# Kernel optimization log

Hardware: AMD Instinct MI355X
Metric: run time of the kernel (lower is better)

The kernel has to match this reference:

```python
import jax, jax.numpy as jnp
import numpy as np

B, S, D, H, DFF = 4, 2048, 768, 12, 3072
DH = D // H  # 64
EPS = 1e-5
SQRT_DK = float(np.sqrt(DH))


def layer_norm(x, gamma, beta):
    mu = jnp.mean(x, axis=-1, keepdims=True)
    var = jnp.mean((x - mu) ** 2, axis=-1, keepdims=True)
    return (x - mu) / jnp.sqrt(var + EPS) * gamma + beta


def attention_block(x, Wq, Wv, gamma, beta, mask):
    # NOTE: faithful to source quirks: k and v BOTH come from the V projection
    # (self.K is unused), and softmax is over dim=2 (the QUERY axis) as in
    # nn.Softmax(dim=2) applied to a (B, H, Sq, Sk) tensor.
    b, s, d = x.shape
    q = (x @ Wq).reshape(b, s, H, DH).transpose(0, 2, 1, 3)   # (B,H,S,DH)
    kv = (x @ Wv).reshape(b, s, H, DH).transpose(0, 2, 1, 3)  # (B,H,S,DH)
    w = jnp.einsum('bhqd,bhkd->bhqk', q, kv) / SQRT_DK        # (B,H,S,S)
    w = jnp.where(mask, -1e9, w)
    score = jax.nn.softmax(w, axis=2)  # dim=2 quirk (query axis)
    o = jnp.einsum('bhqk,bhkd->bhqd', score, kv)
    o = o.transpose(0, 2, 1, 3).reshape(b, s, d)
    return layer_norm(o + x, gamma, beta)


def feed_forward(x, W1, b1, W2, b2, gamma, beta):
    h = jax.nn.relu(x @ W1 + b1)
    return layer_norm(h @ W2 + b2 + x, gamma, beta)


def setup_inputs() -> dict:
    key = jax.random.key(0)
    ks = jax.random.split(key, 12)
    std = 1.0 / np.sqrt(D)
    x = jax.random.normal(ks[0], (B, S, D), dtype=jnp.float32)
    # causal mask: True = masked
    mask = jnp.triu(jnp.ones((S, S), dtype=bool), k=1)[None, None]
    return {
        'x': x,
        'mask': mask,
        'Wq1': jax.random.normal(ks[1], (D, D), jnp.float32) * std,
        'Wv1': jax.random.normal(ks[2], (D, D), jnp.float32) * std,
        'g1': jnp.ones((D,), jnp.float32),
        'be1': jnp.zeros((D,), jnp.float32),
        'Wq2': jax.random.normal(ks[3], (D, D), jnp.float32) * std,
        'Wv2': jax.random.normal(ks[4], (D, D), jnp.float32) * std,
        'g2': jnp.ones((D,), jnp.float32),
        'be2': jnp.zeros((D,), jnp.float32),
        'Wf1': jax.random.normal(ks[5], (D, DFF), jnp.float32) * std,
        'bf1': jnp.zeros((DFF,), jnp.float32),
        'Wf2': jax.random.normal(ks[6], (DFF, D), jnp.float32) * (1.0 / np.sqrt(DFF)),
        'bf2': jnp.zeros((D,), jnp.float32),
        'gf': jnp.ones((D,), jnp.float32),
        'bef': jnp.zeros((D,), jnp.float32),
    }


def reference(x, mask, Wq1, Wv1, g1, be1, Wq2, Wv2, g2, be2,
              Wf1, bf1, Wf2, bf2, gf, bef):
    x = attention_block(x, Wq1, Wv1, g1, be1, mask)
    # second block: mask is zeroed in the source (no masking)
    x = attention_block(x, Wq2, Wv2, g2, be2, jnp.zeros_like(mask))
    x = feed_forward(x, Wf1, bf1, Wf2, bf2, gf, bef)
    return x
```

## Files before the change

### kernel.cpp

```cpp
#include <hip/hip_runtime.h>

typedef __attribute__((ext_vector_type(8))) short short8;
typedef __attribute__((ext_vector_type(4))) float floatx4;
typedef __attribute__((ext_vector_type(4))) unsigned short ushort4v;

#define H_ 12
#define S_ 2048
#define D_ 768
#define DFF_ 3072
#define DH_ 64
#define BH_ 48
#define M_ 8192

__device__ __forceinline__ unsigned short f2bf(float f) {
  union { float f; unsigned int u; } a; a.f = f;
  return (unsigned short)((a.u + 0x7FFFu + ((a.u >> 16) & 1u)) >> 16);
}
__device__ __forceinline__ float bf2f(unsigned short s) {
  union { unsigned int u; float f; } a; a.u = ((unsigned int)s) << 16;
  return a.f;
}

__device__ __forceinline__ void glds16(const void* g, void* l) {
  __builtin_amdgcn_global_load_lds(
      (const __attribute__((address_space(1))) void*)(unsigned long long)(size_t)g,
      (__attribute__((address_space(3))) void*)(unsigned int)(size_t)l, 16, 0, 0);
}

__device__ __forceinline__ int swz8(int lin, int nwg) {
  return (lin & 7) * (nwg >> 3) + (lin >> 3);
}

__global__ __launch_bounds__(256) void cvt_bf16(const float* __restrict__ in,
                                                unsigned short* __restrict__ out) {
  size_t i = ((size_t)blockIdx.x * 256 + threadIdx.x) * 4;
  floatx4 v = *reinterpret_cast<const floatx4*>(in + i);
  ushort4v o;
  o[0] = f2bf(v[0]); o[1] = f2bf(v[1]); o[2] = f2bf(v[2]); o[3] = f2bf(v[3]);
  *reinterpret_cast<ushort4v*>(out + i) = o;
}

__global__ __launch_bounds__(256) void wtrans(const float* __restrict__ W,
                                              unsigned short* __restrict__ Wt,
                                              int K, int N) {
  __shared__ float t[64][65];
  const int n0 = blockIdx.x * 64, k0 = blockIdx.y * 64;
  const int tid = threadIdx.x;
#pragma unroll
  for (int i = 0; i < 16; ++i) {
    int idx = tid + 256 * i;
    int kl = idx >> 6, nl = idx & 63;
    t[kl][nl] = W[(size_t)(k0 + kl) * N + n0 + nl];
  }
  __syncthreads();
#pragma unroll
  for (int i = 0; i < 16; ++i) {
    int idx = tid + 256 * i;
    int nl = idx >> 6, kl = idx & 63;
    Wt[(size_t)(n0 + nl) * K + k0 + kl] = f2bf(t[kl][nl]);
  }
}

__global__ __launch_bounds__(256) void kvtrans(const unsigned short* __restrict__ KVb,
                                               unsigned short* __restrict__ KVTb) {
  __shared__ unsigned short t[64][72];
  const int kk0 = blockIdx.x * 64;
  const int bh = blockIdx.y, b = bh / H_, h = bh % H_;
  const size_t xbase = ((size_t)b * S_) * D_ + h * DH_;
  const int tid = threadIdx.x;
#pragma unroll
  for (int i = 0; i < 16; ++i) {
    int idx = tid + 256 * i;
    int kl = idx >> 6, d = idx & 63;
    t[kl][d] = KVb[xbase + (size_t)(kk0 + kl) * D_ + d];
  }
  __syncthreads();
  const size_t tb = (size_t)bh * DH_ * S_;
#pragma unroll
  for (int i = 0; i < 16; ++i) {
    int idx = tid + 256 * i;
    int d = idx >> 6, kl = idx & 63;
    KVTb[tb + (size_t)d * S_ + kk0 + kl] = t[kl][d];
  }
}

template <int EPI, int OUTBF>
__global__ __launch_bounds__(256, 2) void gemm128(const unsigned short* __restrict__ A,
                                                  const unsigned short* __restrict__ Bt,
                                                  const float* __restrict__ bias,
                                                  float scale, void* __restrict__ C0,
                                                  void* __restrict__ C1,
                                                  int M, int N, int K, int lda) {
  __shared__ unsigned short As[128 * 64];
  __shared__ unsigned short Bs[128 * 64];
  const int tid = threadIdx.x;
  const int l = tid & 63, w = tid >> 6;
  const int wm = w >> 1, wn = w & 1;
  const int lrow = l & 15, lk = l >> 4;
  int lin = (blockIdx.z * gridDim.y + blockIdx.y) * gridDim.x + blockIdx.x;
  int nwg = gridDim.x * gridDim.y * gridDim.z;
  int s = swz8(lin, nwg);
  int xt = s % gridDim.x;
  int rest = s / gridDim.x;
  int yt = rest % gridDim.y;
  int zt = rest / gridDim.y;
  const unsigned short* Ao = A + (size_t)zt * K;
  const unsigned short* Bo = Bt + (size_t)zt * K;
  const int m0 = yt * 128, n0 = xt * 128;
  floatx4 acc[4][4] = {};
  for (int k0 = 0; k0 < K; k0 += 64) {
    __syncthreads();
#pragma unroll
    for (int i = 0; i < 4; ++i) {
      int idx = w * 64 + i * 256 + l;
      int row = idx >> 3, c8 = idx & 7;
      int sc = (c8 ^ (row & 7)) << 3;
      glds16(Ao + (size_t)(m0 + row) * lda + k0 + sc, As + (size_t)(w * 64 + i * 256) * 8);
      glds16(Bo + (size_t)(n0 + row) * lda + k0 + sc, Bs + (size_t)(w * 64 + i * 256) * 8);
    }
    __syncthreads();
#pragma unroll
    for (int ks = 0; ks < 2; ++ks) {
      short8 af[4], bfr[4];
#pragma unroll
      for (int f = 0; f < 4; ++f) {
        int ar = wm * 64 + f * 16 + lrow;
        af[f] = *reinterpret_cast<const short8*>(
            &As[ar * 64 + (((ks * 4 + lk) ^ (ar & 7)) << 3)]);
        int br = wn * 64 + f * 16 + lrow;
        bfr[f] = *reinterpret_cast<const short8*>(
            &Bs[br * 64 + (((ks * 4 + lk) ^ (br & 7)) << 3)]);
      }
#pragma unroll
      for (int fm = 0; fm < 4; ++fm)
#pragma unroll
        for (int fn = 0; fn < 4; ++fn)
          acc[fm][fn] =
              __builtin_amdgcn_mfma_f32_16x16x32_bf16(af[fm], bfr[fn], acc[fm][fn], 0, 0, 0);
    }
  }
#pragma unroll
  for (int fm = 0; fm < 4; ++fm) {
#pragma unroll
    for (int fn = 0; fn < 4; ++fn) {
      int col = n0 + wn * 64 + fn * 16 + lrow;
#pragma unroll
      for (int r = 0; r < 4; ++r) {
        int row = m0 + wm * 64 + fm * 16 + lk * 4 + r;
        float v = acc[fm][fn][r];
        if (EPI == 3) {
          if (col < 768)
            ((unsigned short*)C0)[(size_t)row * 768 + col] = f2bf(v * scale);
          else
            ((unsigned short*)C1)[(size_t)row * 768 + col - 768] = f2bf(v);
        } else {
          v = v * scale + ((EPI > 0) ? bias[col] : 0.0f);
          if (EPI == 1) v = fmaxf(v, 0.0f);
          void* Cz = zt ? C1 : C0;
          if (OUTBF) ((unsigned short*)Cz)[(size_t)row * N + col] = f2bf(v);
          else ((float*)Cz)[(size_t)row * N + col] = v;
        }
      }
    }
  }
}

template <bool CAUSAL>
__global__ __launch_bounds__(256, 4) void colsum(const unsigned short* __restrict__ Qb,
                                                 const unsigned short* __restrict__ KVb,
                                                 float* __restrict__ lnl) {
  __shared__ unsigned short kvs[64 * 64];
  __shared__ float lred[4][64];
  const int tid = threadIdx.x;
  const int l = tid & 63, w = tid >> 6;
  const int lrow = l & 15, lk = l >> 4;
  const int sw = swz8(blockIdx.x, 32 * BH_);
  const int bh = sw >> 5, kt = sw & 31;
  const int kk0 = kt * 64;
  const int b = bh / H_, h = bh % H_;
  const size_t xbase = ((size_t)b * S_) * D_ + h * DH_;
#pragma unroll
  for (int i = 0; i < 2; ++i) {
    int idx = w * 64 + i * 256 + l;
    int row = idx >> 3, c8 = idx & 7;
    glds16(KVb + xbase + (size_t)(kk0 + row) * D_ + ((c8 ^ (row & 7)) << 3),
           kvs + (size_t)(w * 64 + i * 256) * 8);
  }
  __syncthreads();
  short8 bkv[4][2];
#pragma unroll
  for (int kkf = 0; kkf < 4; ++kkf)
#pragma unroll
    for (int s = 0; s < 2; ++s) {
      int br = kkf * 16 + lrow;
      bkv[kkf][s] = *reinterpret_cast<const short8*>(
          &kvs[br * 64 + (((s * 4 + lk) ^ (br & 7)) << 3)]);
    }
  float lrun[4] = {0.0f, 0.0f, 0.0f, 0.0f};
  const int qbase = CAUSAL ? kk0 : 0;
  const int ntiles = (S_ - qbase) >> 4;
  for (int t = w; t < ntiles; t += 4) {
    const int q0 = qbase + t * 16;
    const bool maskt = CAUSAL && (q0 < kk0 + 64);
    short8 aq[2];
#pragma unroll
    for (int s = 0; s < 2; ++s)
      aq[s] = *reinterpret_cast<const short8*>(
          &Qb[xbase + (size_t)(q0 + lrow) * D_ + s * 32 + lk * 8]);
#pragma unroll
    for (int kkf = 0; kkf < 4; ++kkf) {
      floatx4 sf = {};
      sf = __builtin_amdgcn_mfma_f32_16x16x32_bf16(aq[0], bkv[kkf][0], sf, 0, 0, 0);
      sf = __builtin_amdgcn_mfma_f32_16x16x32_bf16(aq[1], bkv[kkf][1], sf, 0, 0, 0);
      const int kkg = kk0 + kkf * 16 + lrow;
      float lacc = 0.0f;
      if (maskt) {
#pragma unroll
        for (int r = 0; r < 4; ++r) {
          int qg = q0 + lk * 4 + r;
          lacc += (kkg <= qg) ? __expf(sf[r]) : 0.0f;
        }
      } else {
#pragma unroll
        for (int r = 0; r < 4; ++r) lacc += __expf(sf[r]);
      }
      lrun[kkf] += lacc;
    }
  }
#pragma unroll
  for (int kkf = 0; kkf < 4; ++kkf) {
    float lv = lrun[kkf];
    lv += __shfl_xor(lv, 16, 64);
    lv += __shfl_xor(lv, 32, 64);
    if (l < 16) lred[w][kkf * 16 + l] = lv;
  }
  __syncthreads();
  if (tid < 64) {
    float lv = lred[0][tid] + lred[1][tid] + lred[2][tid] + lred[3][tid];
    lnl[(size_t)bh * S_ + kk0 + tid] = __logf(lv);
  }
}

template <bool CAUSAL>
__global__ __launch_bounds__(256, 4) void attnpv(const unsigned short* __restrict__ Qb,
                                                 const unsigned short* __restrict__ KVb,
                                                 const unsigned short* __restrict__ KVTb,
                                                 const float* __restrict__ lnl,
                                                 float* __restrict__ Opre) {
  __shared__ unsigned short kvs[64 * 64];
  __shared__ unsigned short kvts[64 * 64];
  __shared__ unsigned short ps[4][32 * 64];
  __shared__ float slnl[64];
  const int tid = threadIdx.x;
  const int l = tid & 63, w = tid >> 6;
  const int lrow = l & 15, lk = l >> 4;
  const int sw = swz8(blockIdx.x, 16 * BH_);
  const int bh = sw >> 4, qtr = sw & 15;
  const int qt = CAUSAL ? (15 - qtr) : qtr;
  const int q0 = qt * 128;
  const int wr = w * 32;
  const int b = bh / H_, h = bh % H_;
  const size_t xbase = ((size_t)b * S_) * D_ + h * DH_;
  const size_t tbase = (size_t)bh * DH_ * S_;
  short8 aq[2][2];
#pragma unroll
  for (int fm = 0; fm < 2; ++fm)
#pragma unroll
    for (int s = 0; s < 2; ++s)
      aq[fm][s] = *reinterpret_cast<const short8*>(
          &Qb[xbase + (size_t)(q0 + wr + fm * 16 + lrow) * D_ + s * 32 + lk * 8]);
  floatx4 ao[2][4] = {};
  const int nkk = CAUSAL ? 2 * (qt + 1) : (S_ / 64);
  for (int t = 0; t < nkk; ++t) {
    const int kk0 = t * 64;
    __syncthreads();
#pragma unroll
    for (int i = 0; i < 2; ++i) {
      int idx = w * 64 + i * 256 + l;
      int row = idx >> 3, c8 = idx & 7;
      int sc = (c8 ^ (row & 7)) << 3;
      glds16(KVb + xbase + (size_t)(kk0 + row) * D_ + sc,
             kvs + (size_t)(w * 64 + i * 256) * 8);
      glds16(KVTb + tbase + (size_t)row * S_ + kk0 + sc,
             kvts + (size_t)(w * 64 + i * 256) * 8);
    }
    if (tid < 64) slnl[tid] = lnl[(size_t)bh * S_ + kk0 + tid];
    __syncthreads();
    const bool maskt = CAUSAL && (kk0 + 64 > q0);
#pragma unroll
    for (int kkf = 0; kkf < 4; ++kkf) {
      const int kkl = kkf * 16 + lrow;
      const int br = kkf * 16 + lrow;
      short8 b0 = *reinterpret_cast<const short8*>(&kvs[br * 64 + ((lk ^ (br & 7)) << 3)]);
      short8 b1 =
          *reinterpret_cast<const short8*>(&kvs[br * 64 + (((4 + lk) ^ (br & 7)) << 3)]);
      const float nl = -slnl[kkl];
      const int kkg = kk0 + kkl;
#pragma unroll
      for (int fm = 0; fm < 2; ++fm) {
        floatx4 sf = {nl, nl, nl, nl};
        sf = __builtin_amdgcn_mfma_f32_16x16x32_bf16(aq[fm][0], b0, sf, 0, 0, 0);
        sf = __builtin_amdgcn_mfma_f32_16x16x32_bf16(aq[fm][1], b1, sf, 0, 0, 0);
#pragma unroll
        for (int r = 0; r < 4; ++r) {
          int prow = fm * 16 + lk * 4 + r;
          float p;
          if (maskt)
            p = (kkg <= q0 + wr + prow) ? __expf(sf[r]) : 0.0f;
          else
            p = __expf(sf[r]);
          ps[w][prow * 64 + (((kkl >> 3) ^ (prow & 7)) << 3) + (kkl & 7)] = f2bf(p);
        }
      }
    }
    short8 pa[2][2];
#pragma unroll
    for (int fm = 0; fm < 2; ++fm)
#pragma unroll
      for (int s2 = 0; s2 < 2; ++s2)
        pa[fm][s2] = *reinterpret_cast<const short8*>(
            &ps[w][(fm * 16 + lrow) * 64 + (((s2 * 4 + lk) ^ (lrow & 7)) << 3)]);
#pragma unroll
    for (int dn = 0; dn < 4; ++dn) {
#pragma unroll
      for (int s2 = 0; s2 < 2; ++s2) {
        const int br2 = dn * 16 + lrow;
        short8 bv = *reinterpret_cast<const short8*>(
            &kvts[br2 * 64 + (((s2 * 4 + lk) ^ (br2 & 7)) << 3)]);
#pragma unroll
        for (int fm = 0; fm < 2; ++fm)
          ao[fm][dn] = __builtin_amdgcn_mfma_f32_16x16x32_bf16(pa[fm][s2], bv, ao[fm][dn], 0, 0, 0);
      }
    }
  }
#pragma unroll
  for (int fm = 0; fm < 2; ++fm)
#pragma unroll
    for (int dn = 0; dn < 4; ++dn)
#pragma unroll
      for (int r = 0; r < 4; ++r)
        Opre[xbase + (size_t)(q0 + wr + fm * 16 + lk * 4 + r) * D_ + dn * 16 + lrow] =
            ao[fm][dn][r];
}

template <bool WRITEBF, bool TWO, bool BIAS>
__global__ __launch_bounds__(256) void ln_kernel(const float* __restrict__ pre,
                                                 const float* __restrict__ pre2,
                                                 const float* __restrict__ bias,
                                                 const float* __restrict__ res,
                                                 const float* __restrict__ gam,
                                                 const float* __restrict__ bet,
                                                 float* __restrict__ outf,
                                                 unsigned short* __restrict__ outb) {
  __shared__ float red[8];
  const int tid = threadIdx.x;
  const size_t base = (size_t)blockIdx.x * D_;
  float v[3];
  float s = 0.0f;
#pragma unroll
  for (int j = 0; j < 3; ++j) {
    int i = tid + 256 * j;
    float t = pre[base + i] + res[base + i];
    if (TWO) t += pre2[base + i];
    if (BIAS) t += bias[i];
    v[j] = t;
    s += t;
  }
#pragma unroll
  for (int off = 32; off; off >>= 1) s += __shfl_xor(s, off, 64);
  if ((tid & 63) == 0) red[tid >> 6] = s;
  __syncthreads();
  s = red[0] + red[1] + red[2] + red[3];
  const float mu = s * (1.0f / 768.0f);
  float vs = 0.0f;
#pragma unroll
  for (int j = 0; j < 3; ++j) { float d = v[j] - mu; vs += d * d; }
#pragma unroll
  for (int off = 32; off; off >>= 1) vs += __shfl_xor(vs, off, 64);
  if ((tid & 63) == 0) red[4 + (tid >> 6)] = vs;
  __syncthreads();
  vs = red[4] + red[5] + red[6] + red[7];
  const float rstd = rsqrtf(vs * (1.0f / 768.0f) + 1e-5f);
#pragma unroll
  for (int j = 0; j < 3; ++j) {
    int i = tid + 256 * j;
    float o = (v[j] - mu) * rstd * gam[i] + bet[i];
    outf[base + i] = o;
    if (WRITEBF) outb[base + i] = f2bf(o);
  }
}

extern "C" void kernel_launch(void* const* d_in, const int* in_sizes, int n_in,
                              void* d_out, int out_size, void* d_ws, size_t ws_size,
                              hipStream_t stream) {
  const float* x = (const float*)d_in[0];
  const float* Wq1 = (const float*)d_in[2];
  const float* Wv1 = (const float*)d_in[3];
  const float* g1 = (const float*)d_in[4];
  const float* be1 = (const float*)d_in[5];
  const float* Wq2 = (const float*)d_in[6];
  const float* Wv2 = (const float*)d_in[7];
  const float* g2 = (const float*)d_in[8];
  const float* be2 = (const float*)d_in[9];
  const float* Wf1 = (const float*)d_in[10];
  const float* bf1 = (const float*)d_in[11];
  const float* Wf2 = (const float*)d_in[12];
  const float* bf2 = (const float*)d_in[13];
  const float* gf = (const float*)d_in[14];
  const float* bef = (const float*)d_in[15];

  char* ws = (char*)d_ws;
  size_t off = 0;
  auto alloc = [&](size_t bytes) -> void* {
    void* p = ws + off;
    off += (bytes + 255) & ~(size_t)255;
    return p;
  };
  unsigned short* xb = (unsigned short*)alloc((size_t)M_ * D_ * 2);
  unsigned short* qb = (unsigned short*)alloc((size_t)M_ * D_ * 2);
  unsigned short* kvb = (unsigned short*)alloc((size_t)M_ * D_ * 2);
  unsigned short* kvtb = (unsigned short*)alloc((size_t)BH_ * DH_ * S_ * 2);
  float* lnl = (float*)alloc((size_t)BH_ * S_ * 4);
  float* preA = (float*)alloc((size_t)M_ * D_ * 4);
  float* xcur = (float*)alloc((size_t)M_ * D_ * 4);
  unsigned short* hb = (unsigned short*)alloc((size_t)M_ * DFF_ * 2);
  unsigned short* wqv1t = (unsigned short*)alloc((size_t)D_ * 1536 * 2);
  unsigned short* wqv2t = (unsigned short*)alloc((size_t)D_ * 1536 * 2);
  unsigned short* wf1t = (unsigned short*)alloc((size_t)D_ * DFF_ * 2);
  unsigned short* wf2t = (unsigned short*)alloc((size_t)D_ * DFF_ * 2);
  float* preB = (float*)qb;
  if (off > ws_size) return;

  const dim3 blk(256);
  cvt_bf16<<<dim3((M_ * D_) / 1024), blk, 0, stream>>>(x, xb);
  wtrans<<<dim3(12, 12), blk, 0, stream>>>(Wq1, wqv1t, D_, D_);
  wtrans<<<dim3(12, 12), blk, 0, stream>>>(Wv1, wqv1t + (size_t)768 * 768, D_, D_);
  wtrans<<<dim3(12, 12), blk, 0, stream>>>(Wq2, wqv2t, D_, D_);
  wtrans<<<dim3(12, 12), blk, 0, stream>>>(Wv2, wqv2t + (size_t)768 * 768, D_, D_);
  wtrans<<<dim3(48, 12), blk, 0, stream>>>(Wf1, wf1t, D_, DFF_);
  wtrans<<<dim3(12, 48), blk, 0, stream>>>(Wf2, wf2t, DFF_, D_);

  const dim3 gqkv(12, 64);
  const dim3 gkvt(S_ / 64, BH_);

  gemm128<3, 1><<<gqkv, blk, 0, stream>>>(xb, wqv1t, nullptr, 0.125f, qb, kvb, M_, 1536, D_, D_);
  kvtrans<<<gkvt, blk, 0, stream>>>(kvb, kvtb);
  colsum<true><<<dim3(32 * BH_), blk, 0, stream>>>(qb, kvb, lnl);
  attnpv<true><<<dim3(16 * BH_), blk, 0, stream>>>(qb, kvb, kvtb, lnl, preA);
  ln_kernel<true, false, false><<<dim3(M_), blk, 0, stream>>>(preA, nullptr, nullptr, x, g1,
                                                              be1, xcur, xb);

  gemm128<3, 1><<<gqkv, blk, 0, stream>>>(xb, wqv2t, nullptr, 0.125f, qb, kvb, M_, 1536, D_, D_);
  kvtrans<<<gkvt, blk, 0, stream>>>(kvb, kvtb);
  colsum<false><<<dim3(32 * BH_), blk, 0, stream>>>(qb, kvb, lnl);
  attnpv<false><<<dim3(16 * BH_), blk, 0, stream>>>(qb, kvb, kvtb, lnl, preA);
  ln_kernel<true, false, false><<<dim3(M_), blk, 0, stream>>>(preA, nullptr, nullptr, xcur, g2,
                                                              be2, xcur, xb);

  gemm128<1, 1><<<dim3(24, 64), blk, 0, stream>>>(xb, wf1t, bf1, 1.0f, hb, nullptr, M_, DFF_,
                                                  D_, D_);
  gemm128<0, 0><<<dim3(6, 64, 2), blk, 0, stream>>>(hb, wf2t, nullptr, 1.0f, preA, preB, M_, D_,
                                                    DFF_ / 2, DFF_);
  ln_kernel<false, true, true><<<dim3(M_), blk, 0, stream>>>(preA, preB, bf2, xcur, gf, bef,
                                                             (float*)d_out, nullptr);
}
```

Baseline: 565.5 us.

## Load K/V fragments directly from global in attnpv, prefetch Q in lse kernel

The PV attention kernel stops staging K/V and K/V-transposed tiles and log-normalizers through shared memory with block barriers. Each wave now reads its MFMA operand fragments straight from global memory (relying on L2/L1 reuse across the four waves), and the occupancy hint is lowered from 4 to 3 blocks per SM to allow more registers. Separately, the row-normalizer kernel software-prefetches the next Q tile into registers while computing the current one. This removes two barriers per iteration and the LDS traffic, at the cost of four times redundant global loads and lower occupancy.

```diff
diff --git a/kernel.cpp b/kernel.cpp
--- a/kernel.cpp
+++ b/kernel.cpp
@@ -15,10 +15,6 @@
 __device__ __forceinline__ unsigned short f2bf(float f) {
   union { float f; unsigned int u; } a; a.f = f;
   return (unsigned short)((a.u + 0x7FFFu + ((a.u >> 16) & 1u)) >> 16);
-}
-__device__ __forceinline__ float bf2f(unsigned short s) {
-  union { unsigned int u; float f; } a; a.u = ((unsigned int)s) << 16;
-  return a.f;
 }
 
 __device__ __forceinline__ void glds16(const void* g, void* l) {
@@ -199,19 +195,30 @@
   float lrun[4] = {0.0f, 0.0f, 0.0f, 0.0f};
   const int qbase = CAUSAL ? kk0 : 0;
   const int ntiles = (S_ - qbase) >> 4;
+  short8 aqn[2];
+  if (w < ntiles) {
+    const int q0 = qbase + w * 16;
+#pragma unroll
+    for (int s = 0; s < 2; ++s)
+      aqn[s] = *reinterpret_cast<const short8*>(
+          &Qb[xbase + (size_t)(q0 + lrow) * D_ + s * 32 + lk * 8]);
+  }
   for (int t = w; t < ntiles; t += 4) {
     const int q0 = qbase + t * 16;
     const bool maskt = CAUSAL && (q0 < kk0 + 64);
-    short8 aq[2];
-#pragma unroll
-    for (int s = 0; s < 2; ++s)
-      aq[s] = *reinterpret_cast<const short8*>(
-          &Qb[xbase + (size_t)(q0 + lrow) * D_ + s * 32 + lk * 8]);
+    short8 aq0 = aqn[0], aq1 = aqn[1];
+    if (t + 4 < ntiles) {
+      const int qn = qbase + (t + 4) * 16;
+#pragma unroll
+      for (int s = 0; s < 2; ++s)
+        aqn[s] = *reinterpret_cast<const short8*>(
+            &Qb[xbase + (size_t)(qn + lrow) * D_ + s * 32 + lk * 8]);
+    }
 #pragma unroll
     for (int kkf = 0; kkf < 4; ++kkf) {
       floatx4 sf = {};
-      sf = __builtin_amdgcn_mfma_f32_16x16x32_bf16(aq[0], bkv[kkf][0], sf, 0, 0, 0);
-      sf = __builtin_amdgcn_mfma_f32_16x16x32_bf16(aq[1], bkv[kkf][1], sf, 0, 0, 0);
+      sf = __builtin_amdgcn_mfma_f32_16x16x32_bf16(aq0, bkv[kkf][0], sf, 0, 0, 0);
+      sf = __builtin_amdgcn_mfma_f32_16x16x32_bf16(aq1, bkv[kkf][1], sf, 0, 0, 0);
       const int kkg = kk0 + kkf * 16 + lrow;
       float lacc = 0.0f;
       if (maskt) {
@@ -242,15 +249,12 @@
 }
 
 template <bool CAUSAL>
-__global__ __launch_bounds__(256, 4) void attnpv(const unsigned short* __restrict__ Qb,
+__global__ __launch_bounds__(256, 3) void attnpv(const unsigned short* __restrict__ Qb,
                                                  const unsigned short* __restrict__ KVb,
                                                  const unsigned short* __restrict__ KVTb,
                                                  const float* __restrict__ lnl,
                                                  float* __restrict__ Opre) {
-  __shared__ unsigned short kvs[64 * 64];
-  __shared__ unsigned short kvts[64 * 64];
   __shared__ unsigned short ps[4][32 * 64];
-  __shared__ float slnl[64];
   const int tid = threadIdx.x;
   const int l = tid & 63, w = tid >> 6;
   const int lrow = l & 15, lk = l >> 4;
@@ -262,6 +266,7 @@
   const int b = bh / H_, h = bh % H_;
   const size_t xbase = ((size_t)b * S_) * D_ + h * DH_;
   const size_t tbase = (size_t)bh * DH_ * S_;
+  const float* lnlb = lnl + (size_t)bh * S_;
   short8 aq[2][2];
 #pragma unroll
   for (int fm = 0; fm < 2; ++fm)
@@ -273,28 +278,24 @@
   const int nkk = CAUSAL ? 2 * (qt + 1) : (S_ / 64);
   for (int t = 0; t < nkk; ++t) {
     const int kk0 = t * 64;
-    __syncthreads();
-#pragma unroll
-    for (int i = 0; i < 2; ++i) {
-      int idx = w * 64 + i * 256 + l;
-      int row = idx >> 3, c8 = idx & 7;
-      int sc = (c8 ^ (row & 7)) << 3;
-      glds16(KVb + xbase + (size_t)(kk0 + row) * D_ + sc,
-             kvs + (size_t)(w * 64 + i * 256) * 8);
-      glds16(KVTb + tbase + (size_t)row * S_ + kk0 + sc,
-             kvts + (size_t)(w * 64 + i * 256) * 8);
-    }
-    if (tid < 64) slnl[tid] = lnl[(size_t)bh * S_ + kk0 + tid];
-    __syncthreads();
     const bool maskt = CAUSAL && (kk0 + 64 > q0);
+    short8 bv[4][2];
+#pragma unroll
+    for (int dn = 0; dn < 4; ++dn)
+#pragma unroll
+      for (int s2 = 0; s2 < 2; ++s2)
+        bv[dn][s2] = *reinterpret_cast<const short8*>(
+            &KVTb[tbase + (size_t)(dn * 16 + lrow) * S_ + kk0 + s2 * 32 + lk * 8]);
+    float nls[4];
+#pragma unroll
+    for (int kkf = 0; kkf < 4; ++kkf) nls[kkf] = lnlb[kk0 + kkf * 16 + lrow];
 #pragma unroll
     for (int kkf = 0; kkf < 4; ++kkf) {
       const int kkl = kkf * 16 + lrow;
-      const int br = kkf * 16 + lrow;
-      short8 b0 = *reinterpret_cast<const short8*>(&kvs[br * 64 + ((lk ^ (br & 7)) << 3)]);
-      short8 b1 =
-          *reinterpret_cast<const short8*>(&kvs[br * 64 + (((4 + lk) ^ (br & 7)) << 3)]);
-      const float nl = -slnl[kkl];
+      const unsigned short* kr = &KVb[xbase + (size_t)(kk0 + kkl) * D_];
+      short8 b0 = *reinterpret_cast<const short8*>(kr + lk * 8);
+      short8 b1 = *reinterpret_cast<const short8*>(kr + 32 + lk * 8);
+      const float nl = -nls[kkf];
       const int kkg = kk0 + kkl;
 #pragma unroll
       for (int fm = 0; fm < 2; ++fm) {
@@ -321,17 +322,13 @@
         pa[fm][s2] = *reinterpret_cast<const short8*>(
             &ps[w][(fm * 16 + lrow) * 64 + (((s2 * 4 + lk) ^ (lrow & 7)) << 3)]);
 #pragma unroll
-    for (int dn = 0; dn < 4; ++dn) {
-#pragma unroll
-      for (int s2 = 0; s2 < 2; ++s2) {
-        const int br2 = dn * 16 + lrow;
-        short8 bv = *reinterpret_cast<const short8*>(
-            &kvts[br2 * 64 + (((s2 * 4 + lk) ^ (br2 & 7)) << 3)]);
+    for (int dn = 0; dn < 4; ++dn)
+#pragma unroll
+      for (int s2 = 0; s2 < 2; ++s2)
 #pragma unroll
         for (int fm = 0; fm < 2; ++fm)
-          ao[fm][dn] = __builtin_amdgcn_mfma_f32_16x16x32_bf16(pa[fm][s2], bv, ao[fm][dn], 0, 0, 0);
-      }
-    }
+          ao[fm][dn] =
+              __builtin_amdgcn_mfma_f32_16x16x32_bf16(pa[fm][s2], bv[dn][s2], ao[fm][dn], 0, 0, 0);
   }
 #pragma unroll
   for (int fm = 0; fm < 2; ++fm)
```

Result: slower. 703.8 us (+24.5%).

## Double-buffer KV tiles in attnpv with async LDS loads and setprio

Applied to the files above, without the earlier changes.

Converts the attnpv kernel's K/V and log-normalizer staging to a double-buffered pipeline. The next tile is issued with global_load_lds while the current tile is computed, and the code waits with explicit vmcnt counts and raw s_barrier. The log-normalizer load becomes a direct-to-LDS 4-byte load replicated per wave, and MFMA priority is raised around the PV loop. Doubling LDS use lowers the occupancy hint from 4 to 3 blocks per CU, trading occupancy for latency hiding.

```diff
diff --git a/kernel.cpp b/kernel.cpp
--- a/kernel.cpp
+++ b/kernel.cpp
@@ -16,15 +16,16 @@
   union { float f; unsigned int u; } a; a.f = f;
   return (unsigned short)((a.u + 0x7FFFu + ((a.u >> 16) & 1u)) >> 16);
 }
-__device__ __forceinline__ float bf2f(unsigned short s) {
-  union { unsigned int u; float f; } a; a.u = ((unsigned int)s) << 16;
-  return a.f;
-}
 
 __device__ __forceinline__ void glds16(const void* g, void* l) {
   __builtin_amdgcn_global_load_lds(
       (const __attribute__((address_space(1))) void*)(unsigned long long)(size_t)g,
       (__attribute__((address_space(3))) void*)(unsigned int)(size_t)l, 16, 0, 0);
+}
+__device__ __forceinline__ void glds4(const void* g, void* l) {
+  __builtin_amdgcn_global_load_lds(
+      (const __attribute__((address_space(1))) void*)(unsigned long long)(size_t)g,
+      (__attribute__((address_space(3))) void*)(unsigned int)(size_t)l, 4, 0, 0);
 }
 
 __device__ __forceinline__ int swz8(int lin, int nwg) {
@@ -242,15 +243,15 @@
 }
 
 template <bool CAUSAL>
-__global__ __launch_bounds__(256, 4) void attnpv(const unsigned short* __restrict__ Qb,
+__global__ __launch_bounds__(256, 3) void attnpv(const unsigned short* __restrict__ Qb,
                                                  const unsigned short* __restrict__ KVb,
                                                  const unsigned short* __restrict__ KVTb,
                                                  const float* __restrict__ lnl,
                                                  float* __restrict__ Opre) {
-  __shared__ unsigned short kvs[64 * 64];
-  __shared__ unsigned short kvts[64 * 64];
+  __shared__ unsigned short kvs[2][64 * 64];
+  __shared__ unsigned short kvts[2][64 * 64];
+  __shared__ float slnl[2][4][64];
   __shared__ unsigned short ps[4][32 * 64];
-  __shared__ float slnl[64];
   const int tid = threadIdx.x;
   const int l = tid & 63, w = tid >> 6;
   const int lrow = l & 15, lk = l >> 4;
@@ -262,6 +263,23 @@
   const int b = bh / H_, h = bh % H_;
   const size_t xbase = ((size_t)b * S_) * D_ + h * DH_;
   const size_t tbase = (size_t)bh * DH_ * S_;
+  const float* lnlb = lnl + (size_t)bh * S_;
+
+  auto STAGE = [&](int buf, int t) {
+    const int kk0 = t * 64;
+#pragma unroll
+    for (int i = 0; i < 2; ++i) {
+      int idx = w * 64 + i * 256 + l;
+      int row = idx >> 3, c8 = idx & 7;
+      int sc = (c8 ^ (row & 7)) << 3;
+      glds16(KVb + xbase + (size_t)(kk0 + row) * D_ + sc,
+             &kvs[buf][(size_t)(w * 64 + i * 256) * 8]);
+      glds16(KVTb + tbase + (size_t)row * S_ + kk0 + sc,
+             &kvts[buf][(size_t)(w * 64 + i * 256) * 8]);
+    }
+    glds4(lnlb + kk0 + l, &slnl[buf][w][0]);
+  };
+
   short8 aq[2][2];
 #pragma unroll
   for (int fm = 0; fm < 2; ++fm)
@@ -271,30 +289,31 @@
           &Qb[xbase + (size_t)(q0 + wr + fm * 16 + lrow) * D_ + s * 32 + lk * 8]);
   floatx4 ao[2][4] = {};
   const int nkk = CAUSAL ? 2 * (qt + 1) : (S_ / 64);
+
+  STAGE(0, 0);
+  int cur = 0;
   for (int t = 0; t < nkk; ++t) {
     const int kk0 = t * 64;
-    __syncthreads();
-#pragma unroll
-    for (int i = 0; i < 2; ++i) {
-      int idx = w * 64 + i * 256 + l;
-      int row = idx >> 3, c8 = idx & 7;
-      int sc = (c8 ^ (row & 7)) << 3;
-      glds16(KVb + xbase + (size_t)(kk0 + row) * D_ + sc,
-             kvs + (size_t)(w * 64 + i * 256) * 8);
-      glds16(KVTb + tbase + (size_t)row * S_ + kk0 + sc,
-             kvts + (size_t)(w * 64 + i * 256) * 8);
-    }
-    if (tid < 64) slnl[tid] = lnl[(size_t)bh * S_ + kk0 + tid];
-    __syncthreads();
     const bool maskt = CAUSAL && (kk0 + 64 > q0);
+    if (t + 1 < nkk) {
+      STAGE(cur ^ 1, t + 1);
+      __builtin_amdgcn_sched_barrier(0);
+      asm volatile("s_waitcnt vmcnt(5)" ::: "memory");
+    } else {
+      __builtin_amdgcn_sched_barrier(0);
+      asm volatile("s_waitcnt vmcnt(0)" ::: "memory");
+    }
+    __builtin_amdgcn_s_barrier();
+    __builtin_amdgcn_sched_barrier(0);
 #pragma unroll
     for (int kkf = 0; kkf < 4; ++kkf) {
       const int kkl = kkf * 16 + lrow;
       const int br = kkf * 16 + lrow;
-      short8 b0 = *reinterpret_cast<const short8*>(&kvs[br * 64 + ((lk ^ (br & 7)) << 3)]);
+      short8 b0 =
+          *reinterpret_cast<const short8*>(&kvs[cur][br * 64 + ((lk ^ (br & 7)) << 3)]);
       short8 b1 =
-          *reinterpret_cast<const short8*>(&kvs[br * 64 + (((4 + lk) ^ (br & 7)) << 3)]);
-      const float nl = -slnl[kkl];
+          *reinterpret_cast<const short8*>(&kvs[cur][br * 64 + (((4 + lk) ^ (br & 7)) << 3)]);
+      const float nl = -slnl[cur][w][kkl];
       const int kkg = kk0 + kkl;
 #pragma unroll
       for (int fm = 0; fm < 2; ++fm) {
@@ -320,18 +339,25 @@
       for (int s2 = 0; s2 < 2; ++s2)
         pa[fm][s2] = *reinterpret_cast<const short8*>(
             &ps[w][(fm * 16 + lrow) * 64 + (((s2 * 4 + lk) ^ (lrow & 7)) << 3)]);
+    __builtin_amdgcn_s_setprio(1);
 #pragma unroll
     for (int dn = 0; dn < 4; ++dn) {
 #pragma unroll
       for (int s2 = 0; s2 < 2; ++s2) {
         const int br2 = dn * 16 + lrow;
         short8 bv = *reinterpret_cast<const short8*>(
-            &kvts[br2 * 64 + (((s2 * 4 + lk) ^ (br2 & 7)) << 3)]);
+            &kvts[cur][br2 * 64 + (((s2 * 4 + lk) ^ (br2 & 7)) << 3)]);
 #pragma unroll
         for (int fm = 0; fm < 2; ++fm)
-          ao[fm][dn] = __builtin_amdgcn_mfma_f32_16x16x32_bf16(pa[fm][s2], bv, ao[fm][dn], 0, 0, 0);
+          ao[fm][dn] =
+              __builtin_amdgcn_mfma_f32_16x16x32_bf16(pa[fm][s2], bv, ao[fm][dn], 0, 0, 0);
       }
     }
+    __builtin_amdgcn_s_setprio(0);
+    __builtin_amdgcn_sched_barrier(0);
+    __builtin_amdgcn_s_barrier();
+    __builtin_amdgcn_sched_barrier(0);
+    cur ^= 1;
   }
 #pragma unroll
   for (int fm = 0; fm < 2; ++fm)
```

After: 516.8 us. 1.09x faster.
